# Optimization experiments

Hardware: AMD Instinct MI355X
Metric: run time of the kernel (lower is better)

Reference implementation:

```python
import jax, jax.numpy as jnp
import numpy as np


def setup_inputs() -> dict:
    key = jax.random.key(0)
    k1, k2 = jax.random.split(key)
    B, H, V, N = 256, 4096, 1024, 32
    v = jax.random.uniform(k1, (B, V, N), dtype=jnp.float32)
    W = jax.random.normal(k2, (H, V, N), dtype=jnp.float32) / np.sqrt(V * N + 2)
    b_h = jnp.zeros((H,), dtype=jnp.float32)
    b_v = jnp.zeros((V, N), dtype=jnp.float32)
    return {"v": v, "W": W, "b_h": b_h, "b_v": b_v}


def reference(v, W, b_h, b_v):
    # (v.unsqueeze(-3) * W).sum([-1,-2]) is a contraction over (visible, category):
    # einsum 'bvn,hvn->bh' — a GEMM with K = n_visible * n.
    logits = jnp.einsum('bvn,hvn->bh', v, W) + b_h          # [B, H]
    sp = jax.nn.softplus(logits).sum(-1)                     # [B]
    vt = jnp.einsum('bvn,vn->b', v, b_v)                     # [B]
    return sp + vt
```

## Files before the change

### kernel.cpp

```cpp
#include <hip/hip_runtime.h>
#include <hip/hip_bf16.h>
#include <stdint.h>

#define B_ 256
#define H_ 4096
#define K_ 32768

typedef __attribute__((ext_vector_type(8))) short bf16x8;
typedef __attribute__((ext_vector_type(4))) float f32x4;

__device__ __forceinline__ unsigned short f2bf(float x) {
    union { float f; unsigned int u; } c; c.f = x;
    unsigned int r = c.u + 0x7FFFu + ((c.u >> 16) & 1u);
    return (unsigned short)(r >> 16);
}

__device__ __forceinline__ short bfc(float x) {
    __hip_bfloat16 h = __float2bfloat16(x);
    union { __hip_bfloat16 h; short s; } c; c.h = h;
    return c.s;
}

__device__ __forceinline__ float softplus_f(float x) {
    return fmaxf(x, 0.0f) + log1pf(expf(-fabsf(x)));
}

__global__ __launch_bounds__(256) void prep_kernel(
    const float* __restrict__ v, const float* __restrict__ bv,
    __hip_bfloat16* __restrict__ vbf, float* __restrict__ vt)
{
    const int b = blockIdx.x;
    const int t = threadIdx.x;
    const float* vr = v + (size_t)b * K_;
    unsigned short* dr = (unsigned short*)(vbf + (size_t)b * K_);
    float acc = 0.f;
    for (int i = t * 8; i < K_; i += 256 * 8) {
        float4 x0 = *(const float4*)(vr + i);
        float4 x1 = *(const float4*)(vr + i + 4);
        float4 b0 = *(const float4*)(bv + i);
        float4 b1 = *(const float4*)(bv + i + 4);
        acc += x0.x*b0.x + x0.y*b0.y + x0.z*b0.z + x0.w*b0.w
             + x1.x*b1.x + x1.y*b1.y + x1.z*b1.z + x1.w*b1.w;
        ushort4 u0, u1;
        u0.x = f2bf(x0.x); u0.y = f2bf(x0.y); u0.z = f2bf(x0.z); u0.w = f2bf(x0.w);
        u1.x = f2bf(x1.x); u1.y = f2bf(x1.y); u1.z = f2bf(x1.z); u1.w = f2bf(x1.w);
        *(ushort4*)(dr + i)     = u0;
        *(ushort4*)(dr + i + 4) = u1;
    }
    __shared__ float sm[256];
    sm[t] = acc;
    __syncthreads();
    for (int s = 128; s > 0; s >>= 1) {
        if (t < s) sm[t] += sm[t + s];
        __syncthreads();
    }
    if (t == 0) vt[b] = sm[0];
}


#define NCONS 8

#define LOAD_A(dst, kt) do {                                                           \
    _Pragma("unroll")                                                                  \
    for (int m_ = 0; m_ < 2; ++m_)                                                     \
      _Pragma("unroll")                                                                \
      for (int s_ = 0; s_ < 2; ++s_)                                                   \
        dst[m_*2+s_] = *(const bf16x8*)(ap[m_] + (size_t)(kt) * 64 + s_ * 32);         \
    } while (0)

#define COMPUTE(AUSE, T_) do {                                                         \
    const unsigned short* wb_ = &wtile[(T_) & 3][0];                                   \
    _Pragma("unroll")                                                                  \
    for (int s_ = 0; s_ < 2; ++s_) {                                                   \
      bf16x8 bfr[4];                                                                   \
      _Pragma("unroll")                                                                \
      for (int n_ = 0; n_ < 4; ++n_) {                                                 \
        int row_  = n_ * 16 + lr;                                                      \
        int slot_ = s_ * 4 + lg;                                                       \
        bfr[n_] = *(const bf16x8*)&wb_[row_ * 64 + ((slot_ ^ (row_ & 7)) << 3)];       \
      }                                                                                \
      _Pragma("unroll")                                                                \
      for (int m_ = 0; m_ < 2; ++m_)                                                   \
        _Pragma("unroll")                                                              \
        for (int n_ = 0; n_ < 4; ++n_)                                                 \
          acc[m_][n_] = __builtin_amdgcn_mfma_f32_16x16x32_bf16(                       \
              AUSE[m_*2+s_], bfr[n_], acc[m_][n_], 0, 0, 0);                           \
    } } while (0)

#define CBODY(T_, AUSE, ALOAD, ISSA, VMSTR) do {                                       \
    if (ISSA) LOAD_A(ALOAD, (T_) + 1);                                                 \
    asm volatile("s_waitcnt " VMSTR ::: "memory");                                     \
    COMPUTE(AUSE, T_);                                                                 \
    asm volatile("s_barrier" ::: "memory");                                            \
    } while (0)

#define PLOAD(dst, kt) do {                                                            \
    _Pragma("unroll")                                                                  \
    for (int c_ = 0; c_ < 4; ++c_) {                                                   \
        const float* p_ = wsrc4[c_] + (size_t)(kt) * 64;                               \
        dst[c_*2]   = *(const float4*)p_;                                              \
        dst[c_*2+1] = *(const float4*)(p_ + 4);                                        \
    } } while (0)

#define PWRITE(src, slot_) do {                                                        \
    _Pragma("unroll")                                                                  \
    for (int c_ = 0; c_ < 4; ++c_) {                                                   \
        bf16x8 u_;                                                                     \
        u_[0]=bfc(src[c_*2].x);   u_[1]=bfc(src[c_*2].y);                              \
        u_[2]=bfc(src[c_*2].z);   u_[3]=bfc(src[c_*2].w);                              \
        u_[4]=bfc(src[c_*2+1].x); u_[5]=bfc(src[c_*2+1].y);                            \
        u_[6]=bfc(src[c_*2+1].z); u_[7]=bfc(src[c_*2+1].w);                            \
        *(bf16x8*)&wtile[(slot_)][woff4[c_]] = u_;                                     \
    } } while (0)

#define PBODY(T_, LBUF, WBUF) do {                                                     \
    PLOAD(LBUF, (T_) + 2);                                                             \
    asm volatile("s_waitcnt vmcnt(8)" ::: "memory");                                   \
    PWRITE(WBUF, ((T_) + 1) & 3);                                                      \
    asm volatile("s_waitcnt lgkmcnt(0)\n\ts_barrier" ::: "memory");                    \
    } while (0)

__global__ __launch_bounds__(640, 5) void gemm_kernel(
    const __hip_bfloat16* __restrict__ vbf,
    const float* __restrict__ W,
    float* __restrict__ part,
    int KS, int NT)
{
    __shared__ __align__(16) unsigned short wtile[4][64 * 64];

    const int tid  = threadIdx.x;
    const int wid  = tid >> 6;
    const int lane = tid & 63;
    const int lr   = lane & 15;
    const int lg   = lane >> 4;

    const int bid   = blockIdx.x;
    const int sidx  = bid % KS;
    const int ht    = bid / KS;
    const int h0    = ht * 64;
    const int kbase = sidx * (NT * 64);

    if (wid < NCONS) {
        const __hip_bfloat16* ap[2];
        #pragma unroll
        for (int m = 0; m < 2; ++m)
            ap[m] = vbf + (size_t)(wid * 32 + m * 16 + lr) * K_ + kbase + lg * 8;

        f32x4 acc[2][4];
        #pragma unroll
        for (int m = 0; m < 2; ++m)
            #pragma unroll
            for (int n = 0; n < 4; ++n)
                acc[m][n] = (f32x4)(0.0f);

        bf16x8 aA[4], aB[4];
        LOAD_A(aA, 0);
        asm volatile("s_barrier" ::: "memory");

        for (int t = 0; t < NT - 2; t += 2) {
            CBODY(t,     aA, aB, true, "vmcnt(4)");
            CBODY(t + 1, aB, aA, true, "vmcnt(4)");
        }
        CBODY(NT - 2, aA, aB, true,  "vmcnt(4)");
        CBODY(NT - 1, aB, aA, false, "vmcnt(0)");

        float* pout = part + (size_t)sidx * ((size_t)B_ * H_) + h0;
        #pragma unroll
        for (int m = 0; m < 2; ++m)
            #pragma unroll
            for (int n = 0; n < 4; ++n)
                #pragma unroll
                for (int j = 0; j < 4; ++j) {
                    int brow = wid * 32 + m * 16 + lg * 4 + j;
                    int hcol = n * 16 + lr;
                    pout[(size_t)brow * H_ + hcol] = acc[m][n][j];
                }
    } else {
        const int pw = wid - NCONS;
        const float* wsrc4[4];
        int woff4[4];
        #pragma unroll
        for (int c = 0; c < 4; ++c) {
            int idx = c * 128 + pw * 64 + lane;
            int row = idx >> 3;
            int c8  = idx & 7;
            wsrc4[c] = W + (size_t)(h0 + row) * K_ + kbase + c8 * 8;
            woff4[c] = row * 64 + ((c8 ^ (row & 7)) << 3);
        }

        float4 wgA[8], wgB[8];
        PLOAD(wgA, 0);
        PLOAD(wgB, 1);
        asm volatile("s_waitcnt vmcnt(8)" ::: "memory");
        PWRITE(wgA, 0);
        asm volatile("s_waitcnt lgkmcnt(0)\n\ts_barrier" ::: "memory");

        for (int t = 0; t < NT - 2; t += 2) {
            PBODY(t,     wgA, wgB);
            PBODY(t + 1, wgB, wgA);
        }
        asm volatile("s_waitcnt vmcnt(0)" ::: "memory");
        PWRITE(wgB, (NT - 1) & 3);
        asm volatile("s_waitcnt lgkmcnt(0)\n\ts_barrier" ::: "memory");
        asm volatile("s_barrier" ::: "memory");
    }
}

__global__ __launch_bounds__(256) void reduce_kernel(
    const float* __restrict__ part, const float* __restrict__ bh,
    const float* __restrict__ vt, float* __restrict__ out, int KS)
{
    const int b = blockIdx.x;
    const int t = threadIdx.x;
    float sp = 0.f;
    const float* pb = part + (size_t)b * H_;
    for (int h = t * 4; h < H_; h += 256 * 4) {
        float4 l = *(const float4*)(bh + h);
        for (int s = 0; s < KS; ++s) {
            float4 p = *(const float4*)(pb + (size_t)s * B_ * H_ + h);
            l.x += p.x; l.y += p.y; l.z += p.z; l.w += p.w;
        }
        sp += softplus_f(l.x) + softplus_f(l.y) + softplus_f(l.z) + softplus_f(l.w);
    }
    __shared__ float sm[256];
    sm[t] = sp;
    __syncthreads();
    for (int r = 128; r > 0; r >>= 1) {
        if (t < r) sm[t] += sm[t + r];
        __syncthreads();
    }
    if (t == 0) out[b] = sm[0] + vt[b];
}

extern "C" void kernel_launch(void* const* d_in, const int* in_sizes, int n_in,
                              void* d_out, int out_size, void* d_ws, size_t ws_size,
                              hipStream_t stream)
{
    const float* v  = (const float*)d_in[0];
    const float* W  = (const float*)d_in[1];
    const float* bh = (const float*)d_in[2];
    const float* bv = (const float*)d_in[3];
    float* out = (float*)d_out;

    char* ws = (char*)d_ws;
    const size_t vbf_bytes = (size_t)B_ * K_ * sizeof(__hip_bfloat16);
    __hip_bfloat16* vbf = (__hip_bfloat16*)ws;

    int KS = 8;
    while (KS > 1 && vbf_bytes + (size_t)KS * B_ * H_ * 4 + 1024 > ws_size) KS >>= 1;

    float* part = (float*)(ws + vbf_bytes);
    float* vt   = (float*)(ws + vbf_bytes + (size_t)KS * B_ * H_ * 4);

    prep_kernel<<<B_, 256, 0, stream>>>(v, bv, vbf, vt);
    const int NT = (K_ / KS) / 64;
    gemm_kernel<<<(H_ / 64) * KS, 640, 0, stream>>>(vbf, W, part, KS, NT);
    reduce_kernel<<<B_, 256, 0, stream>>>(part, bh, vt, out, KS);
}
```

Baseline: 206.3 us.

## Batch W producer stages four quarter-tiles per barrier with eight-slot LDS ring

Each producer lane now loads 32 contiguous floats (a quarter-tile of 16 rows) per issue, where before it loaded strided 8-float chunks. It writes four quarter-tiles per barrier into an 8-slot LDS ring, so consumers sync once every four k-steps instead of every step. This cuts barrier overhead and improves global load contiguity per lane. In exchange LDS per block doubles to 64KB, which may lower occupancy, and the barrier protocol between producer and consumer indexing has to stay matched.

```diff
diff --git a/kernel.cpp b/kernel.cpp
--- a/kernel.cpp
+++ b/kernel.cpp
@@ -69,7 +69,7 @@
     } while (0)
 
 #define COMPUTE(AUSE, T_) do {                                                         \
-    const unsigned short* wb_ = &wtile[(T_) & 3][0];                                   \
+    const unsigned short* wb_ = &wtile[(T_) & 7][0];                                   \
     _Pragma("unroll")                                                                  \
     for (int s_ = 0; s_ < 2; ++s_) {                                                   \
       bf16x8 bfr[4];                                                                   \
@@ -91,34 +91,29 @@
     if (ISSA) LOAD_A(ALOAD, (T_) + 1);                                                 \
     asm volatile("s_waitcnt " VMSTR ::: "memory");                                     \
     COMPUTE(AUSE, T_);                                                                 \
-    asm volatile("s_barrier" ::: "memory");                                            \
     } while (0)
 
-#define PLOAD(dst, kt) do {                                                            \
-    _Pragma("unroll")                                                                  \
-    for (int c_ = 0; c_ < 4; ++c_) {                                                   \
-        const float* p_ = wsrc4[c_] + (size_t)(kt) * 64;                               \
-        dst[c_*2]   = *(const float4*)p_;                                              \
-        dst[c_*2+1] = *(const float4*)(p_ + 4);                                        \
+#define PISS(dst, Q_) do {                                                             \
+    const float* p_ = wlanebase + (size_t)((Q_) >> 2) * 256                            \
+                                + (size_t)((Q_) & 3) * 16 * K_;                        \
+    _Pragma("unroll")                                                                  \
+    for (int i_ = 0; i_ < 8; ++i_)                                                     \
+        dst[i_] = *(const float4*)(p_ + i_ * 4);                                       \
+    } while (0)
+
+#define PWRITE(src, Q_) do {                                                           \
+    int base_ = ((((Q_) & ~3) + jj) & 7) * 4096 + (((Q_) & 3) * 16 + pr) * 64;        \
+    _Pragma("unroll")                                                                  \
+    for (int u_ = 0; u_ < 4; ++u_) {                                                   \
+        float4 a_ = src[2*u_], b_ = src[2*u_+1];                                       \
+        bf16x8 t_;                                                                     \
+        t_[0]=bfc(a_.x); t_[1]=bfc(a_.y); t_[2]=bfc(a_.z); t_[3]=bfc(a_.w);            \
+        t_[4]=bfc(b_.x); t_[5]=bfc(b_.y); t_[6]=bfc(b_.z); t_[7]=bfc(b_.w);            \
+        *(bf16x8*)&wtile[0][base_ + swzofs[u_]] = t_;                                  \
     } } while (0)
 
-#define PWRITE(src, slot_) do {                                                        \
-    _Pragma("unroll")                                                                  \
-    for (int c_ = 0; c_ < 4; ++c_) {                                                   \
-        bf16x8 u_;                                                                     \
-        u_[0]=bfc(src[c_*2].x);   u_[1]=bfc(src[c_*2].y);                              \
-        u_[2]=bfc(src[c_*2].z);   u_[3]=bfc(src[c_*2].w);                              \
-        u_[4]=bfc(src[c_*2+1].x); u_[5]=bfc(src[c_*2+1].y);                            \
-        u_[6]=bfc(src[c_*2+1].z); u_[7]=bfc(src[c_*2+1].w);                            \
-        *(bf16x8*)&wtile[(slot_)][woff4[c_]] = u_;                                     \
-    } } while (0)
-
-#define PBODY(T_, LBUF, WBUF) do {                                                     \
-    PLOAD(LBUF, (T_) + 2);                                                             \
-    asm volatile("s_waitcnt vmcnt(8)" ::: "memory");                                   \
-    PWRITE(WBUF, ((T_) + 1) & 3);                                                      \
-    asm volatile("s_waitcnt lgkmcnt(0)\n\ts_barrier" ::: "memory");                    \
-    } while (0)
+#define VMW(N) asm volatile("s_waitcnt vmcnt(" #N ")" ::: "memory")
+#define PBAR() asm volatile("s_waitcnt lgkmcnt(0)\n\ts_barrier" ::: "memory")
 
 __global__ __launch_bounds__(640, 5) void gemm_kernel(
     const __hip_bfloat16* __restrict__ vbf,
@@ -126,7 +121,7 @@
     float* __restrict__ part,
     int KS, int NT)
 {
-    __shared__ __align__(16) unsigned short wtile[4][64 * 64];
+    __shared__ __align__(16) unsigned short wtile[8][64 * 64];
 
     const int tid  = threadIdx.x;
     const int wid  = tid >> 6;
@@ -157,10 +152,15 @@
         LOAD_A(aA, 0);
         asm volatile("s_barrier" ::: "memory");
 
-        for (int t = 0; t < NT - 2; t += 2) {
+        for (int t = 0; t < NT - 4; t += 4) {
             CBODY(t,     aA, aB, true, "vmcnt(4)");
             CBODY(t + 1, aB, aA, true, "vmcnt(4)");
+            CBODY(t + 2, aA, aB, true, "vmcnt(4)");
+            CBODY(t + 3, aB, aA, true, "vmcnt(4)");
+            asm volatile("s_barrier" ::: "memory");
         }
+        CBODY(NT - 4, aA, aB, true,  "vmcnt(4)");
+        CBODY(NT - 3, aB, aA, true,  "vmcnt(4)");
         CBODY(NT - 2, aA, aB, true,  "vmcnt(4)");
         CBODY(NT - 1, aB, aA, false, "vmcnt(0)");
 
@@ -177,32 +177,35 @@
                 }
     } else {
         const int pw = wid - NCONS;
-        const float* wsrc4[4];
-        int woff4[4];
-        #pragma unroll
-        for (int c = 0; c < 4; ++c) {
-            int idx = c * 128 + pw * 64 + lane;
-            int row = idx >> 3;
-            int c8  = idx & 7;
-            wsrc4[c] = W + (size_t)(h0 + row) * K_ + kbase + c8 * 8;
-            woff4[c] = row * 64 + ((c8 ^ (row & 7)) << 3);
+        const int m7 = lane >> 3;
+        const int c  = lane & 7;
+        const int jj = c >> 1;
+        const int pr = pw * 8 + m7;
+        const float* wlanebase =
+            W + (size_t)(h0 + pr) * K_ + kbase + c * 32;
+
+        int swzofs[4];
+        #pragma unroll
+        for (int u = 0; u < 4; ++u)
+            swzofs[u] = ((((c & 1) * 4 + u) ^ m7) << 3);
+
+        float4 bufA[8], bufB[8];
+        const int QMAX = NT;
+
+        PISS(bufA, 0);
+        PISS(bufB, 1);
+        for (int Q = 0; Q < QMAX; Q += 4) {
+            VMW(8); PWRITE(bufA, Q);
+            if (Q + 2 < QMAX) PISS(bufA, Q + 2);
+            VMW(8); PWRITE(bufB, Q + 1);
+            if (Q + 3 < QMAX) PISS(bufB, Q + 3);
+            VMW(8); PWRITE(bufA, Q + 2);
+            if (Q + 4 < QMAX) PISS(bufA, Q + 4);
+            if (Q + 4 >= QMAX) { VMW(0); } else { VMW(8); }
+            PWRITE(bufB, Q + 3);
+            if (Q + 5 < QMAX) PISS(bufB, Q + 5);
+            PBAR();
         }
-
-        float4 wgA[8], wgB[8];
-        PLOAD(wgA, 0);
-        PLOAD(wgB, 1);
-        asm volatile("s_waitcnt vmcnt(8)" ::: "memory");
-        PWRITE(wgA, 0);
-        asm volatile("s_waitcnt lgkmcnt(0)\n\ts_barrier" ::: "memory");
-
-        for (int t = 0; t < NT - 2; t += 2) {
-            PBODY(t,     wgA, wgB);
-            PBODY(t + 1, wgB, wgA);
-        }
-        asm volatile("s_waitcnt vmcnt(0)" ::: "memory");
-        PWRITE(wgB, (NT - 1) & 3);
-        asm volatile("s_waitcnt lgkmcnt(0)\n\ts_barrier" ::: "memory");
-        asm volatile("s_barrier" ::: "memory");
     }
 }
 
```

Result: slower. 260.4 us (+26.2%).
